# Optimization experiments

Hardware: AMD Instinct MI355X
Metric: run time of the kernel (lower is better)

Reference implementation:

```python
import jax, jax.numpy as jnp
import numpy as np

INPUT_LENGTH = 1048576
CONF_THRESHOLD = 0.5
# encoding_type == 'CENTER_DURATION'

def setup_inputs() -> dict:
    key = jax.random.key(0)
    yolo_outputs_batch = jax.random.uniform(key, (32, 131072, 8), dtype=jnp.float32)
    return {"yolo_outputs_batch": yolo_outputs_batch}


def reference(yolo_outputs_batch):
    """Decode YOLO-style 1D (audio) detections.

    Original TF layer emits a ragged tensor of only the fragments whose
    confidence passes the threshold (boolean_mask compaction per batch).
    JAX requires static shapes, so we return the dense decoded fragments
    [B, G, F-1] plus the boolean validity mask [B, G]; invalid rows are
    zeroed. Compacting (fragments[b][mask[b]]) reproduces the TF output.
    """
    x = yolo_outputs_batch
    B, G, F = x.shape
    dt = x.dtype
    grid_cells = jnp.arange(G, dtype=dt)[None, :]              # [1, G]
    mask = x[..., 0] >= jnp.asarray(CONF_THRESHOLD, dt)        # [B, G]
    cell_binded_coef = jnp.asarray(INPUT_LENGTH / G, dt)
    cell_unbinded_coef = jnp.asarray(INPUT_LENGTH, dt)
    centers = (grid_cells + x[..., 1]) * cell_binded_coef      # [B, G]
    durations = x[..., 2] * cell_unbinded_coef                 # [B, G]
    # CENTER_DURATION encoding
    starts = jnp.round(centers - durations / 2)
    ends = jnp.round(centers + durations / 2)
    fragments = jnp.concatenate(
        [starts[..., None], ends[..., None], x[..., 3:]], axis=-1
    )                                                           # [B, G, F-1]
    fragments = jnp.where(mask[..., None], fragments, jnp.zeros((), dt))
    return fragments, mask
```

## Files before the change

### kernel.cpp

```cpp
#include <hip/hip_runtime.h>


constexpr int BLOCK = 256;
constexpr int F_OUT = 7;

__global__ __launch_bounds__(BLOCK) void yolo_decode_kernel(
    const float4* __restrict__ in,
    float* __restrict__ frag,
    float* __restrict__ mask_out,
    int g_mask,
    float cell_coef,
    float unbind_coef)
{
    __shared__ float s_frag[BLOCK * F_OUT];

    const int tid       = threadIdx.x;
    const int cell_base = blockIdx.x * BLOCK;
    const int cell      = cell_base + tid;

    const float4 a = in[(size_t)cell * 2];
    const float4 b = in[(size_t)cell * 2 + 1];

    const int   g = cell & g_mask;
    const bool  m = a.x >= 0.5f;

    const float center = __fmul_rn(__fadd_rn((float)g, a.y), cell_coef);
    const float halfd  = __fmul_rn(__fmul_rn(a.z, unbind_coef), 0.5f);
    const float s_val  = rintf(__fadd_rn(center, -halfd));
    const float e_val  = rintf(__fadd_rn(center,  halfd));

    const float o[F_OUT] = { s_val, e_val, a.w, b.x, b.y, b.z, b.w };
    #pragma unroll
    for (int k = 0; k < F_OUT; ++k)
        s_frag[tid * F_OUT + k] = m ? o[k] : 0.0f;

    mask_out[cell] = m ? 1.0f : 0.0f;

    __syncthreads();

    float* dst = frag + (size_t)cell_base * F_OUT;
    #pragma unroll
    for (int k = 0; k < F_OUT; ++k) {
        const int idx = k * BLOCK + tid;
        dst[idx] = s_frag[idx];
    }
}

extern "C" void kernel_launch(void* const* d_in, const int* in_sizes, int n_in,
                              void* d_out, int out_size, void* d_ws, size_t ws_size,
                              hipStream_t stream) {
    (void)n_in; (void)d_ws; (void)ws_size; (void)out_size;

    const float* x   = (const float*)d_in[0];
    float*       out = (float*)d_out;

    constexpr int F_IN        = 8;
    constexpr int G           = 131072;
    constexpr float INPUT_LEN = 1048576.0f;

    const int total_cells = in_sizes[0] / F_IN;
    float* frag = out;
    float* mask = out + (size_t)total_cells * F_OUT;

    const int blocks = total_cells / BLOCK;

    yolo_decode_kernel<<<blocks, BLOCK, 0, stream>>>(
        (const float4*)x, frag, mask,
        G - 1, INPUT_LEN / (float)G, INPUT_LEN);
}
```

Before: 228.1 us.

## Process four cells per thread and write outputs as float4 without shared memory

Each thread now decodes four consecutive cells, which gives it 28 output floats it can write as seven float4 stores, plus one float4 store for the mask. This removes the shared-memory staging buffer and the __syncthreads barrier, and the launch uses a quarter as many blocks. The per-thread stores are strided 112 bytes apart across lanes, so coalescing may be worse than the old fully contiguous scalar stores, and register use goes up. The duration coefficient is also premultiplied by 0.5, which drops one multiply per cell.

```diff
diff --git a/kernel.cpp b/kernel.cpp
--- a/kernel.cpp
+++ b/kernel.cpp
@@ -2,48 +2,58 @@
 
 
 constexpr int BLOCK = 256;
+constexpr int CPT   = 4;
 constexpr int F_OUT = 7;
 
 __global__ __launch_bounds__(BLOCK) void yolo_decode_kernel(
     const float4* __restrict__ in,
-    float* __restrict__ frag,
-    float* __restrict__ mask_out,
+    float4* __restrict__ frag4,
+    float4* __restrict__ mask4,
     int g_mask,
     float cell_coef,
-    float unbind_coef)
+    float half_coef)
 {
-    __shared__ float s_frag[BLOCK * F_OUT];
+    const int t     = blockIdx.x * BLOCK + threadIdx.x;
+    const int cell0 = t * CPT;
 
-    const int tid       = threadIdx.x;
-    const int cell_base = blockIdx.x * BLOCK;
-    const int cell      = cell_base + tid;
+    float4 r[2 * CPT];
+    const float4* p = in + (size_t)cell0 * 2;
+    #pragma unroll
+    for (int i = 0; i < 2 * CPT; ++i) r[i] = p[i];
 
-    const float4 a = in[(size_t)cell * 2];
-    const float4 b = in[(size_t)cell * 2 + 1];
+    const int g0 = cell0 & g_mask;
 
-    const int   g = cell & g_mask;
-    const bool  m = a.x >= 0.5f;
+    float v[CPT * F_OUT];
+    float mk[CPT];
 
-    const float center = __fmul_rn(__fadd_rn((float)g, a.y), cell_coef);
-    const float halfd  = __fmul_rn(__fmul_rn(a.z, unbind_coef), 0.5f);
-    const float s_val  = rintf(__fadd_rn(center, -halfd));
-    const float e_val  = rintf(__fadd_rn(center,  halfd));
+    #pragma unroll
+    for (int c = 0; c < CPT; ++c) {
+        const float4 a = r[2 * c];
+        const float4 b = r[2 * c + 1];
+        const bool  m  = a.x >= 0.5f;
 
-    const float o[F_OUT] = { s_val, e_val, a.w, b.x, b.y, b.z, b.w };
+        const float center = __fmul_rn(__fadd_rn((float)(g0 + c), a.y), cell_coef);
+        const float halfd  = __fmul_rn(a.z, half_coef);
+        const float s_val  = rintf(__fadd_rn(center, -halfd));
+        const float e_val  = rintf(__fadd_rn(center,  halfd));
+
+        v[c * F_OUT + 0] = m ? s_val : 0.0f;
+        v[c * F_OUT + 1] = m ? e_val : 0.0f;
+        v[c * F_OUT + 2] = m ? a.w   : 0.0f;
+        v[c * F_OUT + 3] = m ? b.x   : 0.0f;
+        v[c * F_OUT + 4] = m ? b.y   : 0.0f;
+        v[c * F_OUT + 5] = m ? b.z   : 0.0f;
+        v[c * F_OUT + 6] = m ? b.w   : 0.0f;
+        mk[c] = m ? 1.0f : 0.0f;
+    }
+
+    float4* dst = frag4 + (size_t)t * F_OUT;
     #pragma unroll
     for (int k = 0; k < F_OUT; ++k)
-        s_frag[tid * F_OUT + k] = m ? o[k] : 0.0f;
+        dst[k] = make_float4(v[4 * k + 0], v[4 * k + 1],
+                             v[4 * k + 2], v[4 * k + 3]);
 
-    mask_out[cell] = m ? 1.0f : 0.0f;
-
-    __syncthreads();
-
-    float* dst = frag + (size_t)cell_base * F_OUT;
-    #pragma unroll
-    for (int k = 0; k < F_OUT; ++k) {
-        const int idx = k * BLOCK + tid;
-        dst[idx] = s_frag[idx];
-    }
+    mask4[t] = make_float4(mk[0], mk[1], mk[2], mk[3]);
 }
 
 extern "C" void kernel_launch(void* const* d_in, const int* in_sizes, int n_in,
@@ -62,9 +72,9 @@
     float* frag = out;
     float* mask = out + (size_t)total_cells * F_OUT;
 
-    const int blocks = total_cells / BLOCK;
+    const int blocks = total_cells / (BLOCK * CPT);
 
     yolo_decode_kernel<<<blocks, BLOCK, 0, stream>>>(
-        (const float4*)x, frag, mask,
-        G - 1, INPUT_LEN / (float)G, INPUT_LEN);
+        (const float4*)x, (float4*)frag, (float4*)mask,
+        G - 1, INPUT_LEN / (float)G, INPUT_LEN * 0.5f);
 }
```

After: 235.9 us. 3.4% more time.
